# Performance work log

Measured on AMD Instinct MI355X. Metric: run time of the kernel, lower is better.

Reference implementation:

```python
import jax, jax.numpy as jnp
import numpy as np

N_NODES = 10000
EPS = 1e-5


def _layernorm(x, gamma, beta):
    mu = jnp.mean(x, axis=-1, keepdims=True)
    var = jnp.mean(jnp.square(x - mu), axis=-1, keepdims=True)
    return (x - mu) * jax.lax.rsqrt(var + EPS) * gamma + beta


def _sage_pool_layer(h, src, dst, Wp, bp, Ws, Wn, b, gamma, beta):
    # DGL SAGEConv(aggregator='pool'):
    #   m_u = relu(h_u @ Wp^T + bp); h_neigh[v] = max_{u in N(v)} m_u (0 if no neighbors)
    #   rst = h @ Ws^T + h_neigh @ Wn^T + b
    m = jax.nn.relu(h @ Wp.T + bp)              # [N, d]
    msg = m[src]                                 # [E, d] gather
    agg = jax.ops.segment_max(msg, dst, num_segments=N_NODES)
    agg = jnp.where(jnp.isfinite(agg), agg, 0.0)  # isolated nodes -> 0
    rst = h @ Ws.T + agg @ Wn.T + b
    # gsage_layer: LayerNorm, then Encoder applies relu (dropout inactive in eval)
    return jax.nn.relu(_layernorm(rst, gamma, beta))


def setup_inputs() -> dict:
    key = jax.random.key(0)
    ks = jax.random.split(key, 16)
    d = 256
    E = 320000
    s = 1.0 / np.sqrt(d)
    inp = {
        "h": jax.random.normal(ks[0], (N_NODES, d), dtype=jnp.float32),
        "edge_src": jax.random.randint(ks[1], (E,), 0, N_NODES, dtype=jnp.int32),
        "edge_dst": jax.random.randint(ks[2], (E,), 0, N_NODES, dtype=jnp.int32),
    }
    for li in range(2):
        kk = jax.random.split(ks[3 + li], 3)
        inp[f"Wp{li}"] = jax.random.normal(kk[0], (d, d), dtype=jnp.float32) * s
        inp[f"bp{li}"] = jnp.zeros((d,), jnp.float32)
        inp[f"Ws{li}"] = jax.random.normal(kk[1], (d, d), dtype=jnp.float32) * s
        inp[f"Wn{li}"] = jax.random.normal(kk[2], (d, d), dtype=jnp.float32) * s
        inp[f"b{li}"] = jnp.zeros((d,), jnp.float32)
        inp[f"g{li}"] = jnp.ones((d,), jnp.float32)
        inp[f"be{li}"] = jnp.zeros((d,), jnp.float32)
    return inp


def reference(h, edge_src, edge_dst,
              Wp0, bp0, Ws0, Wn0, b0, g0, be0,
              Wp1, bp1, Ws1, Wn1, b1, g1, be1):
    h = _sage_pool_layer(h, edge_src, edge_dst, Wp0, bp0, Ws0, Wn0, b0, g0, be0)
    h = _sage_pool_layer(h, edge_src, edge_dst, Wp1, bp1, Ws1, Wn1, b1, g1, be1)
    return h
```

## Files before the change

kernel.cpp:

```cpp
#include <hip/hip_runtime.h>

#define D 256
#define CAP 128
#define ASTRIDE 280
#define LN_EPS 1e-5f

typedef short short8 __attribute__((ext_vector_type(8)));
typedef float floatx4 __attribute__((ext_vector_type(4)));

__device__ __forceinline__ unsigned short f2b(float f) {
    union { float f; unsigned int u; } x; x.f = f;
    unsigned int u = x.u + 0x7FFFu + ((x.u >> 16) & 1u);
    return (unsigned short)(u >> 16);
}

__global__ __launch_bounds__(256) void prep_kernel(
    const float* __restrict__ w0, const float* __restrict__ w1,
    const float* __restrict__ w2, const float* __restrict__ w3,
    const float* __restrict__ w4, const float* __restrict__ w5,
    unsigned short* __restrict__ wb,
    const float* __restrict__ h, unsigned short* __restrict__ hb, int nh4,
    int* __restrict__ cnt, unsigned short* __restrict__ mb, int N)
{
    const int blk = blockIdx.x;
    const int tid = threadIdx.x;
    if (blk < 384) {
        const int wsel = blk >> 6;
        const float* src;
        switch (wsel) {
            case 0: src = w0; break; case 1: src = w1; break;
            case 2: src = w2; break; case 3: src = w3; break;
            case 4: src = w4; break; default: src = w5; break;
        }
        const int idx = (blk & 63) * 1024 + tid * 4;
        const float4 v = *(const float4*)(src + idx);
        ushort4 o;
        o.x = f2b(v.x); o.y = f2b(v.y); o.z = f2b(v.z); o.w = f2b(v.w);
        *(ushort4*)(wb + (size_t)wsel * 65536 + idx) = o;
    } else if (blk < 1024) {
        int i = (blk - 384) * 256 + tid;
        const int stride = 640 * 256;
        for (; i < nh4; i += stride) {
            const float4 v = *(const float4*)(h + (size_t)i * 4);
            ushort4 o;
            o.x = f2b(v.x); o.y = f2b(v.y); o.z = f2b(v.z); o.w = f2b(v.w);
            *(ushort4*)(hb + (size_t)i * 4) = o;
        }
    } else if (blk < 1064) {
        const int i = (blk - 1024) * 256 + tid;
        if (i < N) cnt[i] = 0;
    } else {
        mb[(size_t)N * D + tid] = 0;
    }
}

__global__ __launch_bounds__(256) void gemm_relu(
    const unsigned short* __restrict__ A, const unsigned short* __restrict__ W,
    const float* __restrict__ bias, unsigned short* __restrict__ out_b, int N,
    const int* __restrict__ esrc, const int* __restrict__ edst,
    int* __restrict__ cnt, int* __restrict__ csr, int E, int ngemm)
{
    if ((int)blockIdx.x >= ngemm) {
        const int nsb = gridDim.x - ngemm;
        int i = ((int)blockIdx.x - ngemm) * 256 + threadIdx.x;
        const int stride = nsb * 256;
        for (; i < E; i += stride) {
            const int d = edst[i];
            const int pos = atomicAdd(&cnt[d], 1);
            if (pos < CAP) csr[(size_t)d * CAP + pos] = esrc[i];
        }
        return;
    }

    const int tid = threadIdx.x;
    const int wave = tid >> 6;
    const int lane = tid & 63;
    const int quad = lane >> 4;
    const int l16 = lane & 15;
    const int row0 = blockIdx.x * 16;
    const int koff = quad * 8;

    floatx4 acc[4];
#pragma unroll
    for (int t = 0; t < 4; t++) acc[t] = (floatx4)(0.f);

    const unsigned short* aptr = A + (size_t)(row0 + l16) * D + koff;
    const unsigned short* wptr = W + (size_t)(wave * 64 + l16) * D + koff;
#pragma unroll
    for (int k0 = 0; k0 < D; k0 += 32) {
        const short8 av = *(const short8*)(aptr + k0);
        const short8 b0 = *(const short8*)(wptr + k0);
        const short8 b1 = *(const short8*)(wptr + 16 * D + k0);
        const short8 b2 = *(const short8*)(wptr + 32 * D + k0);
        const short8 b3 = *(const short8*)(wptr + 48 * D + k0);
        acc[0] = __builtin_amdgcn_mfma_f32_16x16x32_bf16(av, b0, acc[0], 0, 0, 0);
        acc[1] = __builtin_amdgcn_mfma_f32_16x16x32_bf16(av, b1, acc[1], 0, 0, 0);
        acc[2] = __builtin_amdgcn_mfma_f32_16x16x32_bf16(av, b2, acc[2], 0, 0, 0);
        acc[3] = __builtin_amdgcn_mfma_f32_16x16x32_bf16(av, b3, acc[3], 0, 0, 0);
    }

#pragma unroll
    for (int t = 0; t < 4; t++) {
        const float bcol = bias[wave * 64 + t * 16 + l16];
#pragma unroll
        for (int r = 0; r < 4; r++) {
            const int rg = row0 + quad * 4 + r;
            const int col = wave * 64 + t * 16 + l16;
            out_b[(size_t)rg * D + col] = f2b(fmaxf(acc[t][r] + bcol, 0.f));
        }
    }
}

__global__ __launch_bounds__(256, 3) void gemm_ln_pool(
    const unsigned short* __restrict__ A, const unsigned short* __restrict__ Wself,
    const unsigned short* __restrict__ Wneigh,
    const unsigned short* __restrict__ mpool,
    const int* __restrict__ cnt, const int* __restrict__ csr,
    const float* __restrict__ bias,
    const float* __restrict__ gamma, const float* __restrict__ beta,
    unsigned short* __restrict__ out_b, float* __restrict__ out_f, int N)
{
    __shared__ int idxS[16][CAP];
    __shared__ unsigned short aggS[16 * ASTRIDE];
    __shared__ float redS[4][16], redS2[4][16], muA[16], rsA[16];

    const int tid = threadIdx.x;
    const int wave = tid >> 6;
    const int lane = tid & 63;
    const int quad = lane >> 4;
    const int l16 = lane & 15;
    const int row0 = blockIdx.x * 16;
    const int koff = quad * 8;
    const int rbase = wave * 4;

    int degs[4];
#pragma unroll
    for (int rr = 0; rr < 4; rr++) degs[rr] = min(cnt[row0 + rbase + rr], CAP);
    int P = max(max(degs[0], degs[1]), max(degs[2], degs[3]));
    P = (P + 3) & ~3;
#pragma unroll
    for (int rr = 0; rr < 4; rr++) {
        const int rg = row0 + rbase + rr;
        for (int i = lane; i < P; i += 64)
            idxS[rbase + rr][i] = (i < degs[rr]) ? csr[(size_t)rg * CAP + i] : N;
    }

    floatx4 acc[4];
#pragma unroll
    for (int t = 0; t < 4; t++) acc[t] = (floatx4)(0.f);

    {
        const unsigned short* aptr = A + (size_t)(row0 + l16) * D + koff;
        const unsigned short* wptr = Wself + (size_t)(wave * 64 + l16) * D + koff;
#pragma unroll
        for (int k0 = 0; k0 < D; k0 += 32) {
            const short8 av = *(const short8*)(aptr + k0);
            const short8 b0 = *(const short8*)(wptr + k0);
            const short8 b1 = *(const short8*)(wptr + 16 * D + k0);
            const short8 b2 = *(const short8*)(wptr + 32 * D + k0);
            const short8 b3 = *(const short8*)(wptr + 48 * D + k0);
            acc[0] = __builtin_amdgcn_mfma_f32_16x16x32_bf16(av, b0, acc[0], 0, 0, 0);
            acc[1] = __builtin_amdgcn_mfma_f32_16x16x32_bf16(av, b1, acc[1], 0, 0, 0);
            acc[2] = __builtin_amdgcn_mfma_f32_16x16x32_bf16(av, b2, acc[2], 0, 0, 0);
            acc[3] = __builtin_amdgcn_mfma_f32_16x16x32_bf16(av, b3, acc[3], 0, 0, 0);
        }
    }

    {
        ushort4 mx[4];
#pragma unroll
        for (int rr = 0; rr < 4; rr++) { mx[rr].x = 0; mx[rr].y = 0; mx[rr].z = 0; mx[rr].w = 0; }
        for (int i = 0; i < P; i += 4) {
            ushort4 av[4][4];
#pragma unroll
            for (int rr = 0; rr < 4; rr++) {
#pragma unroll
                for (int u = 0; u < 4; u++) {
                    const int j = idxS[rbase + rr][i + u];
                    av[rr][u] = *(const ushort4*)(mpool + (size_t)j * D + lane * 4);
                }
            }
#pragma unroll
            for (int rr = 0; rr < 4; rr++) {
#pragma unroll
                for (int u = 0; u < 4; u++) {
                    mx[rr].x = (unsigned short)max((int)mx[rr].x, (int)av[rr][u].x);
                    mx[rr].y = (unsigned short)max((int)mx[rr].y, (int)av[rr][u].y);
                    mx[rr].z = (unsigned short)max((int)mx[rr].z, (int)av[rr][u].z);
                    mx[rr].w = (unsigned short)max((int)mx[rr].w, (int)av[rr][u].w);
                }
            }
        }
#pragma unroll
        for (int rr = 0; rr < 4; rr++)
            *(ushort4*)&aggS[(rbase + rr) * ASTRIDE + lane * 4] = mx[rr];
    }
    __syncthreads();

    {
        const unsigned short* wptr = Wneigh + (size_t)(wave * 64 + l16) * D + koff;
#pragma unroll
        for (int k0 = 0; k0 < D; k0 += 32) {
            const short8 av = *(const short8*)&aggS[l16 * ASTRIDE + koff + k0];
            const short8 b0 = *(const short8*)(wptr + k0);
            const short8 b1 = *(const short8*)(wptr + 16 * D + k0);
            const short8 b2 = *(const short8*)(wptr + 32 * D + k0);
            const short8 b3 = *(const short8*)(wptr + 48 * D + k0);
            acc[0] = __builtin_amdgcn_mfma_f32_16x16x32_bf16(av, b0, acc[0], 0, 0, 0);
            acc[1] = __builtin_amdgcn_mfma_f32_16x16x32_bf16(av, b1, acc[1], 0, 0, 0);
            acc[2] = __builtin_amdgcn_mfma_f32_16x16x32_bf16(av, b2, acc[2], 0, 0, 0);
            acc[3] = __builtin_amdgcn_mfma_f32_16x16x32_bf16(av, b3, acc[3], 0, 0, 0);
        }
    }

    float bcol[4];
#pragma unroll
    for (int t = 0; t < 4; t++) bcol[t] = bias[wave * 64 + t * 16 + l16];
#pragma unroll
    for (int t = 0; t < 4; t++)
#pragma unroll
        for (int r = 0; r < 4; r++) acc[t][r] += bcol[t];

#pragma unroll
    for (int r = 0; r < 4; r++) {
        float s = 0.f, s2 = 0.f;
#pragma unroll
        for (int t = 0; t < 4; t++) {
            const float v = acc[t][r];
            s += v; s2 += v * v;
        }
        s += __shfl_xor(s, 1);  s2 += __shfl_xor(s2, 1);
        s += __shfl_xor(s, 2);  s2 += __shfl_xor(s2, 2);
        s += __shfl_xor(s, 4);  s2 += __shfl_xor(s2, 4);
        s += __shfl_xor(s, 8);  s2 += __shfl_xor(s2, 8);
        if (l16 == 0) {
            redS[wave][quad * 4 + r] = s;
            redS2[wave][quad * 4 + r] = s2;
        }
    }
    __syncthreads();
    if (tid < 16) {
        const float S  = redS[0][tid] + redS[1][tid] + redS[2][tid] + redS[3][tid];
        const float S2 = redS2[0][tid] + redS2[1][tid] + redS2[2][tid] + redS2[3][tid];
        const float mu = S * (1.f / D);
        float var = S2 * (1.f / D) - mu * mu;
        var = fmaxf(var, 0.f);
        muA[tid] = mu;
        rsA[tid] = rsqrtf(var + LN_EPS);
    }
    __syncthreads();

    float gcol[4], becol[4];
#pragma unroll
    for (int t = 0; t < 4; t++) {
        gcol[t] = gamma[wave * 64 + t * 16 + l16];
        becol[t] = beta[wave * 64 + t * 16 + l16];
    }
#pragma unroll
    for (int r = 0; r < 4; r++) {
        const int rl = quad * 4 + r;
        const int rg = row0 + rl;
        const float mu = muA[rl];
        const float rs = rsA[rl];
#pragma unroll
        for (int t = 0; t < 4; t++) {
            const int col = wave * 64 + t * 16 + l16;
            float o = (acc[t][r] - mu) * rs * gcol[t] + becol[t];
            o = fmaxf(o, 0.f);
            if (out_f) out_f[(size_t)rg * D + col] = o;
            else       out_b[(size_t)rg * D + col] = f2b(o);
        }
    }
}

extern "C" void kernel_launch(void* const* d_in, const int* in_sizes, int n_in,
                              void* d_out, int out_size, void* d_ws, size_t ws_size,
                              hipStream_t stream) {
    const float* h    = (const float*)d_in[0];
    const int*   esrc = (const int*)d_in[1];
    const int*   edst = (const int*)d_in[2];
    const float* Wp0  = (const float*)d_in[3];
    const float* bp0  = (const float*)d_in[4];
    const float* Ws0  = (const float*)d_in[5];
    const float* Wn0  = (const float*)d_in[6];
    const float* b0   = (const float*)d_in[7];
    const float* g0   = (const float*)d_in[8];
    const float* be0  = (const float*)d_in[9];
    const float* Wp1  = (const float*)d_in[10];
    const float* bp1  = (const float*)d_in[11];
    const float* Ws1  = (const float*)d_in[12];
    const float* Wn1  = (const float*)d_in[13];
    const float* b1   = (const float*)d_in[14];
    const float* g1   = (const float*)d_in[15];
    const float* be1  = (const float*)d_in[16];

    const int N = in_sizes[0] / D;
    const int E = in_sizes[1];
    const size_t ND = (size_t)N * D;

    unsigned short* hb  = (unsigned short*)d_ws;
    unsigned short* mb  = hb + ND;
    unsigned short* h1b = mb + ND + D;
    unsigned short* wb  = h1b + ND;
    int* cnt = (int*)(wb + 6 * 65536);
    int* csr = cnt + N;

    unsigned short* wpb0 = wb + 0 * 65536;
    unsigned short* wsb0 = wb + 1 * 65536;
    unsigned short* wnb0 = wb + 2 * 65536;
    unsigned short* wpb1 = wb + 3 * 65536;
    unsigned short* wsb1 = wb + 4 * 65536;
    unsigned short* wnb1 = wb + 5 * 65536;

    const int gblocks = N / 16;
    const int sblocks = 128;

    prep_kernel<<<1065, 256, 0, stream>>>(Wp0, Ws0, Wn0, Wp1, Ws1, Wn1, wb,
                                          h, hb, (int)(ND / 4), cnt, mb, N);

    gemm_relu<<<gblocks + sblocks, 256, 0, stream>>>(hb, wpb0, bp0, mb, N,
                                                     esrc, edst, cnt, csr, E, gblocks);
    gemm_ln_pool<<<gblocks, 256, 0, stream>>>(hb, wsb0, wnb0, mb, cnt, csr,
                                              b0, g0, be0, h1b, nullptr, N);

    gemm_relu<<<gblocks, 256, 0, stream>>>(h1b, wpb1, bp1, mb, N,
                                           esrc, edst, cnt, csr, 0, gblocks);
    gemm_ln_pool<<<gblocks, 256, 0, stream>>>(h1b, wsb1, wnb1, mb, cnt, csr,
                                              b1, g1, be1, nullptr, (float*)d_out, N);
}
```

Before: 234.9 us.

## Compact CSR to u16, double-buffer neighbor max-pool loads and prefetch GEMM operands

Stores CSR neighbor indices as 16-bit values, which halves CSR write/read traffic and the shared index buffer. The max-pool gather is restructured into two ping-pong register bursts of 4x4 loads, with the first burst issued before the self GEMM so its latency overlaps MFMA work. The GEMM loops get explicit one-step register prefetch of the next operands, and the pooling max uses vector u16 max. It relies on node IDs fitting in 16 bits (N=10000) and raises register pressure, which may reduce occupancy.

```diff
diff --git a/kernel.cpp b/kernel.cpp
--- a/kernel.cpp
+++ b/kernel.cpp
@@ -7,6 +7,18 @@
 
 typedef short short8 __attribute__((ext_vector_type(8)));
 typedef float floatx4 __attribute__((ext_vector_type(4)));
+typedef unsigned short u16x4 __attribute__((ext_vector_type(4)));
+
+__device__ __forceinline__ u16x4 umax4(u16x4 a, u16x4 b) {
+#if __has_builtin(__builtin_elementwise_max)
+    return __builtin_elementwise_max(a, b);
+#else
+    u16x4 r;
+    r.x = a.x > b.x ? a.x : b.x; r.y = a.y > b.y ? a.y : b.y;
+    r.z = a.z > b.z ? a.z : b.z; r.w = a.w > b.w ? a.w : b.w;
+    return r;
+#endif
+}
 
 __device__ __forceinline__ unsigned short f2b(float f) {
     union { float f; unsigned int u; } x; x.f = f;
@@ -58,7 +70,7 @@
     const unsigned short* __restrict__ A, const unsigned short* __restrict__ W,
     const float* __restrict__ bias, unsigned short* __restrict__ out_b, int N,
     const int* __restrict__ esrc, const int* __restrict__ edst,
-    int* __restrict__ cnt, int* __restrict__ csr, int E, int ngemm)
+    int* __restrict__ cnt, unsigned short* __restrict__ csr, int E, int ngemm)
 {
     if ((int)blockIdx.x >= ngemm) {
         const int nsb = gridDim.x - ngemm;
@@ -67,7 +79,7 @@
         for (; i < E; i += stride) {
             const int d = edst[i];
             const int pos = atomicAdd(&cnt[d], 1);
-            if (pos < CAP) csr[(size_t)d * CAP + pos] = esrc[i];
+            if (pos < CAP) csr[(size_t)d * CAP + pos] = (unsigned short)esrc[i];
         }
         return;
     }
@@ -86,17 +98,29 @@
 
     const unsigned short* aptr = A + (size_t)(row0 + l16) * D + koff;
     const unsigned short* wptr = W + (size_t)(wave * 64 + l16) * D + koff;
+
+    short8 a_c  = *(const short8*)(aptr);
+    short8 b_c0 = *(const short8*)(wptr);
+    short8 b_c1 = *(const short8*)(wptr + 16 * D);
+    short8 b_c2 = *(const short8*)(wptr + 32 * D);
+    short8 b_c3 = *(const short8*)(wptr + 48 * D);
 #pragma unroll
     for (int k0 = 0; k0 < D; k0 += 32) {
-        const short8 av = *(const short8*)(aptr + k0);
-        const short8 b0 = *(const short8*)(wptr + k0);
-        const short8 b1 = *(const short8*)(wptr + 16 * D + k0);
-        const short8 b2 = *(const short8*)(wptr + 32 * D + k0);
-        const short8 b3 = *(const short8*)(wptr + 48 * D + k0);
-        acc[0] = __builtin_amdgcn_mfma_f32_16x16x32_bf16(av, b0, acc[0], 0, 0, 0);
-        acc[1] = __builtin_amdgcn_mfma_f32_16x16x32_bf16(av, b1, acc[1], 0, 0, 0);
-        acc[2] = __builtin_amdgcn_mfma_f32_16x16x32_bf16(av, b2, acc[2], 0, 0, 0);
-        acc[3] = __builtin_amdgcn_mfma_f32_16x16x32_bf16(av, b3, acc[3], 0, 0, 0);
+        short8 a_n, b_n0, b_n1, b_n2, b_n3;
+        if (k0 + 32 < D) {
+            a_n  = *(const short8*)(aptr + k0 + 32);
+            b_n0 = *(const short8*)(wptr + k0 + 32);
+            b_n1 = *(const short8*)(wptr + 16 * D + k0 + 32);
+            b_n2 = *(const short8*)(wptr + 32 * D + k0 + 32);
+            b_n3 = *(const short8*)(wptr + 48 * D + k0 + 32);
+        }
+        acc[0] = __builtin_amdgcn_mfma_f32_16x16x32_bf16(a_c, b_c0, acc[0], 0, 0, 0);
+        acc[1] = __builtin_amdgcn_mfma_f32_16x16x32_bf16(a_c, b_c1, acc[1], 0, 0, 0);
+        acc[2] = __builtin_amdgcn_mfma_f32_16x16x32_bf16(a_c, b_c2, acc[2], 0, 0, 0);
+        acc[3] = __builtin_amdgcn_mfma_f32_16x16x32_bf16(a_c, b_c3, acc[3], 0, 0, 0);
+        if (k0 + 32 < D) {
+            a_c = a_n; b_c0 = b_n0; b_c1 = b_n1; b_c2 = b_n2; b_c3 = b_n3;
+        }
     }
 
 #pragma unroll
@@ -115,12 +139,12 @@
     const unsigned short* __restrict__ A, const unsigned short* __restrict__ Wself,
     const unsigned short* __restrict__ Wneigh,
     const unsigned short* __restrict__ mpool,
-    const int* __restrict__ cnt, const int* __restrict__ csr,
+    const int* __restrict__ cnt, const unsigned short* __restrict__ csr,
     const float* __restrict__ bias,
     const float* __restrict__ gamma, const float* __restrict__ beta,
     unsigned short* __restrict__ out_b, float* __restrict__ out_f, int N)
 {
-    __shared__ int idxS[16][CAP];
+    __shared__ unsigned short idxS[16][CAP];
     __shared__ unsigned short aggS[16 * ASTRIDE];
     __shared__ float redS[4][16], redS2[4][16], muA[16], rsA[16];
 
@@ -137,13 +161,37 @@
 #pragma unroll
     for (int rr = 0; rr < 4; rr++) degs[rr] = min(cnt[row0 + rbase + rr], CAP);
     int P = max(max(degs[0], degs[1]), max(degs[2], degs[3]));
-    P = (P + 3) & ~3;
+    const int P8 = (P + 7) & ~7;
 #pragma unroll
     for (int rr = 0; rr < 4; rr++) {
         const int rg = row0 + rbase + rr;
-        for (int i = lane; i < P; i += 64)
-            idxS[rbase + rr][i] = (i < degs[rr]) ? csr[(size_t)rg * CAP + i] : N;
-    }
+        for (int i = lane; i < P8; i += 64)
+            idxS[rbase + rr][i] = (i < degs[rr]) ? csr[(size_t)rg * CAP + i]
+                                                 : (unsigned short)N;
+    }
+
+    const unsigned short* mrow = mpool + lane * 4;
+    u16x4 bufA[4][4], bufB[4][4];
+    u16x4 mx[4];
+#pragma unroll
+    for (int rr = 0; rr < 4; rr++) mx[rr] = (u16x4)(0);
+
+#define LOAD_BURST(buf, i0)                                                     \
+    {                                                                           \
+        _Pragma("unroll") for (int rr = 0; rr < 4; rr++)                        \
+        _Pragma("unroll") for (int u = 0; u < 4; u++)                           \
+            buf[rr][u] = *(const u16x4*)(mrow +                                 \
+                (size_t)idxS[rbase + rr][(i0) + u] * D);                        \
+    }
+#define CONS_BURST(buf)                                                         \
+    {                                                                           \
+        _Pragma("unroll") for (int rr = 0; rr < 4; rr++)                        \
+            mx[rr] = umax4(mx[rr],                                              \
+                umax4(umax4(buf[rr][0], buf[rr][1]),                            \
+                      umax4(buf[rr][2], buf[rr][3])));                          \
+    }
+
+    if (P8 > 0) LOAD_BURST(bufA, 0);
 
     floatx4 acc[4];
 #pragma unroll
@@ -152,64 +200,71 @@
     {
         const unsigned short* aptr = A + (size_t)(row0 + l16) * D + koff;
         const unsigned short* wptr = Wself + (size_t)(wave * 64 + l16) * D + koff;
+        short8 a_c  = *(const short8*)(aptr);
+        short8 b_c0 = *(const short8*)(wptr);
+        short8 b_c1 = *(const short8*)(wptr + 16 * D);
+        short8 b_c2 = *(const short8*)(wptr + 32 * D);
+        short8 b_c3 = *(const short8*)(wptr + 48 * D);
 #pragma unroll
         for (int k0 = 0; k0 < D; k0 += 32) {
-            const short8 av = *(const short8*)(aptr + k0);
-            const short8 b0 = *(const short8*)(wptr + k0);
-            const short8 b1 = *(const short8*)(wptr + 16 * D + k0);
-            const short8 b2 = *(const short8*)(wptr + 32 * D + k0);
-            const short8 b3 = *(const short8*)(wptr + 48 * D + k0);
-            acc[0] = __builtin_amdgcn_mfma_f32_16x16x32_bf16(av, b0, acc[0], 0, 0, 0);
-            acc[1] = __builtin_amdgcn_mfma_f32_16x16x32_bf16(av, b1, acc[1], 0, 0, 0);
-            acc[2] = __builtin_amdgcn_mfma_f32_16x16x32_bf16(av, b2, acc[2], 0, 0, 0);
-            acc[3] = __builtin_amdgcn_mfma_f32_16x16x32_bf16(av, b3, acc[3], 0, 0, 0);
-        }
-    }
-
-    {
-        ushort4 mx[4];
-#pragma unroll
-        for (int rr = 0; rr < 4; rr++) { mx[rr].x = 0; mx[rr].y = 0; mx[rr].z = 0; mx[rr].w = 0; }
-        for (int i = 0; i < P; i += 4) {
-            ushort4 av[4][4];
-#pragma unroll
-            for (int rr = 0; rr < 4; rr++) {
-#pragma unroll
-                for (int u = 0; u < 4; u++) {
-                    const int j = idxS[rbase + rr][i + u];
-                    av[rr][u] = *(const ushort4*)(mpool + (size_t)j * D + lane * 4);
-                }
+            short8 a_n, b_n0, b_n1, b_n2, b_n3;
+            if (k0 + 32 < D) {
+                a_n  = *(const short8*)(aptr + k0 + 32);
+                b_n0 = *(const short8*)(wptr + k0 + 32);
+                b_n1 = *(const short8*)(wptr + 16 * D + k0 + 32);
+                b_n2 = *(const short8*)(wptr + 32 * D + k0 + 32);
+                b_n3 = *(const short8*)(wptr + 48 * D + k0 + 32);
             }
-#pragma unroll
-            for (int rr = 0; rr < 4; rr++) {
-#pragma unroll
-                for (int u = 0; u < 4; u++) {
-                    mx[rr].x = (unsigned short)max((int)mx[rr].x, (int)av[rr][u].x);
-                    mx[rr].y = (unsigned short)max((int)mx[rr].y, (int)av[rr][u].y);
-                    mx[rr].z = (unsigned short)max((int)mx[rr].z, (int)av[rr][u].z);
-                    mx[rr].w = (unsigned short)max((int)mx[rr].w, (int)av[rr][u].w);
-                }
+            acc[0] = __builtin_amdgcn_mfma_f32_16x16x32_bf16(a_c, b_c0, acc[0], 0, 0, 0);
+            acc[1] = __builtin_amdgcn_mfma_f32_16x16x32_bf16(a_c, b_c1, acc[1], 0, 0, 0);
+            acc[2] = __builtin_amdgcn_mfma_f32_16x16x32_bf16(a_c, b_c2, acc[2], 0, 0, 0);
+            acc[3] = __builtin_amdgcn_mfma_f32_16x16x32_bf16(a_c, b_c3, acc[3], 0, 0, 0);
+            if (k0 + 32 < D) {
+                a_c = a_n; b_c0 = b_n0; b_c1 = b_n1; b_c2 = b_n2; b_c3 = b_n3;
             }
         }
-#pragma unroll
-        for (int rr = 0; rr < 4; rr++)
-            *(ushort4*)&aggS[(rbase + rr) * ASTRIDE + lane * 4] = mx[rr];
-    }
+    }
+
+    if (P8 > 0) {
+        LOAD_BURST(bufB, 4);
+        for (int i = 8; i < P8; i += 8) {
+            CONS_BURST(bufA);
+            LOAD_BURST(bufA, i);
+            CONS_BURST(bufB);
+            LOAD_BURST(bufB, i + 4);
+        }
+        CONS_BURST(bufA);
+        CONS_BURST(bufB);
+    }
+#pragma unroll
+    for (int rr = 0; rr < 4; rr++)
+        *(u16x4*)&aggS[(rbase + rr) * ASTRIDE + lane * 4] = mx[rr];
     __syncthreads();
 
     {
         const unsigned short* wptr = Wneigh + (size_t)(wave * 64 + l16) * D + koff;
+        short8 a_c  = *(const short8*)&aggS[l16 * ASTRIDE + koff];
+        short8 b_c0 = *(const short8*)(wptr);
+        short8 b_c1 = *(const short8*)(wptr + 16 * D);
+        short8 b_c2 = *(const short8*)(wptr + 32 * D);
+        short8 b_c3 = *(const short8*)(wptr + 48 * D);
 #pragma unroll
         for (int k0 = 0; k0 < D; k0 += 32) {
-            const short8 av = *(const short8*)&aggS[l16 * ASTRIDE + koff + k0];
-            const short8 b0 = *(const short8*)(wptr + k0);
-            const short8 b1 = *(const short8*)(wptr + 16 * D + k0);
-            const short8 b2 = *(const short8*)(wptr + 32 * D + k0);
-            const short8 b3 = *(const short8*)(wptr + 48 * D + k0);
-            acc[0] = __builtin_amdgcn_mfma_f32_16x16x32_bf16(av, b0, acc[0], 0, 0, 0);
-            acc[1] = __builtin_amdgcn_mfma_f32_16x16x32_bf16(av, b1, acc[1], 0, 0, 0);
-            acc[2] = __builtin_amdgcn_mfma_f32_16x16x32_bf16(av, b2, acc[2], 0, 0, 0);
-            acc[3] = __builtin_amdgcn_mfma_f32_16x16x32_bf16(av, b3, acc[3], 0, 0, 0);
+            short8 a_n, b_n0, b_n1, b_n2, b_n3;
+            if (k0 + 32 < D) {
+                a_n  = *(const short8*)&aggS[l16 * ASTRIDE + koff + k0 + 32];
+                b_n0 = *(const short8*)(wptr + k0 + 32);
+                b_n1 = *(const short8*)(wptr + 16 * D + k0 + 32);
+                b_n2 = *(const short8*)(wptr + 32 * D + k0 + 32);
+                b_n3 = *(const short8*)(wptr + 48 * D + k0 + 32);
+            }
+            acc[0] = __builtin_amdgcn_mfma_f32_16x16x32_bf16(a_c, b_c0, acc[0], 0, 0, 0);
+            acc[1] = __builtin_amdgcn_mfma_f32_16x16x32_bf16(a_c, b_c1, acc[1], 0, 0, 0);
+            acc[2] = __builtin_amdgcn_mfma_f32_16x16x32_bf16(a_c, b_c2, acc[2], 0, 0, 0);
+            acc[3] = __builtin_amdgcn_mfma_f32_16x16x32_bf16(a_c, b_c3, acc[3], 0, 0, 0);
+            if (k0 + 32 < D) {
+                a_c = a_n; b_c0 = b_n0; b_c1 = b_n1; b_c2 = b_n2; b_c3 = b_n3;
+            }
         }
     }
 
@@ -303,7 +358,7 @@
     unsigned short* h1b = mb + ND + D;
     unsigned short* wb  = h1b + ND;
     int* cnt = (int*)(wb + 6 * 65536);
-    int* csr = cnt + N;
+    unsigned short* csr = (unsigned short*)(cnt + N);
 
     unsigned short* wpb0 = wb + 0 * 65536;
     unsigned short* wsb0 = wb + 1 * 65536;
```

After: 237.4 us. About the same (+1.1%).

## Bucket neighbor lists by source chunk with 16-bit indices for pooled gather

Applied to the files above, without the earlier changes.

The per-destination neighbor list is split into four buckets keyed by which 2560-row chunk the source node falls in. Each bucket holds 16-bit source indices instead of 32-bit, and the max-pooling gather walks the buckets in order. This aims to improve cache locality of the gathered message rows and to halve the index storage and traffic. The max reduction is also rewritten with vector elementwise max. In exchange, each bucket is padded separately, which adds extra padded gathers per row group. The scheme also depends on N fitting in 16 bits and on a hardcoded block bound in the prep kernel.

```diff
diff --git a/kernel.cpp b/kernel.cpp
--- a/kernel.cpp
+++ b/kernel.cpp
@@ -1,12 +1,26 @@
 #include <hip/hip_runtime.h>
 
 #define D 256
-#define CAP 128
+#define NCHUNK 4
+#define CHUNK_ROWS 2560
+#define CAP4 64
 #define ASTRIDE 280
 #define LN_EPS 1e-5f
 
 typedef short short8 __attribute__((ext_vector_type(8)));
 typedef float floatx4 __attribute__((ext_vector_type(4)));
+typedef unsigned short u16x4 __attribute__((ext_vector_type(4)));
+
+__device__ __forceinline__ u16x4 umax4(u16x4 a, u16x4 b) {
+#if __has_builtin(__builtin_elementwise_max)
+    return __builtin_elementwise_max(a, b);
+#else
+    u16x4 r;
+    r.x = a.x > b.x ? a.x : b.x; r.y = a.y > b.y ? a.y : b.y;
+    r.z = a.z > b.z ? a.z : b.z; r.w = a.w > b.w ? a.w : b.w;
+    return r;
+#endif
+}
 
 __device__ __forceinline__ unsigned short f2b(float f) {
     union { float f; unsigned int u; } x; x.f = f;
@@ -46,9 +60,9 @@
             o.x = f2b(v.x); o.y = f2b(v.y); o.z = f2b(v.z); o.w = f2b(v.w);
             *(ushort4*)(hb + (size_t)i * 4) = o;
         }
-    } else if (blk < 1064) {
+    } else if (blk < 1181) {
         const int i = (blk - 1024) * 256 + tid;
-        if (i < N) cnt[i] = 0;
+        if (i < N * NCHUNK) cnt[i] = 0;
     } else {
         mb[(size_t)N * D + tid] = 0;
     }
@@ -58,7 +72,7 @@
     const unsigned short* __restrict__ A, const unsigned short* __restrict__ W,
     const float* __restrict__ bias, unsigned short* __restrict__ out_b, int N,
     const int* __restrict__ esrc, const int* __restrict__ edst,
-    int* __restrict__ cnt, int* __restrict__ csr, int E, int ngemm)
+    int* __restrict__ cnt, unsigned short* __restrict__ csr, int E, int ngemm)
 {
     if ((int)blockIdx.x >= ngemm) {
         const int nsb = gridDim.x - ngemm;
@@ -66,8 +80,11 @@
         const int stride = nsb * 256;
         for (; i < E; i += stride) {
             const int d = edst[i];
-            const int pos = atomicAdd(&cnt[d], 1);
-            if (pos < CAP) csr[(size_t)d * CAP + pos] = esrc[i];
+            const int s = esrc[i];
+            const int ch = s / CHUNK_ROWS;
+            const int pos = atomicAdd(&cnt[d * NCHUNK + ch], 1);
+            if (pos < CAP4)
+                csr[((size_t)d * NCHUNK + ch) * CAP4 + pos] = (unsigned short)s;
         }
         return;
     }
@@ -115,12 +132,12 @@
     const unsigned short* __restrict__ A, const unsigned short* __restrict__ Wself,
     const unsigned short* __restrict__ Wneigh,
     const unsigned short* __restrict__ mpool,
-    const int* __restrict__ cnt, const int* __restrict__ csr,
+    const int* __restrict__ cnt, const unsigned short* __restrict__ csr,
     const float* __restrict__ bias,
     const float* __restrict__ gamma, const float* __restrict__ beta,
     unsigned short* __restrict__ out_b, float* __restrict__ out_f, int N)
 {
-    __shared__ int idxS[16][CAP];
+    __shared__ unsigned short idxS[16][NCHUNK][CAP4];
     __shared__ unsigned short aggS[16 * ASTRIDE];
     __shared__ float redS[4][16], redS2[4][16], muA[16], rsA[16];
 
@@ -133,16 +150,22 @@
     const int koff = quad * 8;
     const int rbase = wave * 4;
 
-    int degs[4];
-#pragma unroll
-    for (int rr = 0; rr < 4; rr++) degs[rr] = min(cnt[row0 + rbase + rr], CAP);
-    int P = max(max(degs[0], degs[1]), max(degs[2], degs[3]));
-    P = (P + 3) & ~3;
-#pragma unroll
-    for (int rr = 0; rr < 4; rr++) {
-        const int rg = row0 + rbase + rr;
-        for (int i = lane; i < P; i += 64)
-            idxS[rbase + rr][i] = (i < degs[rr]) ? csr[(size_t)rg * CAP + i] : N;
+    int P4[NCHUNK];
+#pragma unroll
+    for (int ch = 0; ch < NCHUNK; ch++) {
+        int degs[4];
+#pragma unroll
+        for (int rr = 0; rr < 4; rr++)
+            degs[rr] = min(cnt[(row0 + rbase + rr) * NCHUNK + ch], CAP4);
+        int P = max(max(degs[0], degs[1]), max(degs[2], degs[3]));
+        P4[ch] = (P + 3) & ~3;
+#pragma unroll
+        for (int rr = 0; rr < 4; rr++) {
+            const size_t base = ((size_t)(row0 + rbase + rr) * NCHUNK + ch) * CAP4;
+            for (int i = lane; i < P4[ch]; i += 64)
+                idxS[rbase + rr][ch][i] = (i < degs[rr]) ? csr[base + i]
+                                                         : (unsigned short)N;
+        }
     }
 
     floatx4 acc[4];
@@ -167,33 +190,33 @@
     }
 
     {
-        ushort4 mx[4];
-#pragma unroll
-        for (int rr = 0; rr < 4; rr++) { mx[rr].x = 0; mx[rr].y = 0; mx[rr].z = 0; mx[rr].w = 0; }
-        for (int i = 0; i < P; i += 4) {
-            ushort4 av[4][4];
-#pragma unroll
-            for (int rr = 0; rr < 4; rr++) {
-#pragma unroll
-                for (int u = 0; u < 4; u++) {
-                    const int j = idxS[rbase + rr][i + u];
-                    av[rr][u] = *(const ushort4*)(mpool + (size_t)j * D + lane * 4);
+        const unsigned short* mrow = mpool + lane * 4;
+        u16x4 mx[4];
+#pragma unroll
+        for (int rr = 0; rr < 4; rr++) mx[rr] = (u16x4)(0);
+#pragma unroll
+        for (int ch = 0; ch < NCHUNK; ch++) {
+            const int P = P4[ch];
+            for (int i = 0; i < P; i += 4) {
+                u16x4 av[4][4];
+#pragma unroll
+                for (int rr = 0; rr < 4; rr++) {
+#pragma unroll
+                    for (int u = 0; u < 4; u++) {
+                        const int j = idxS[rbase + rr][ch][i + u];
+                        av[rr][u] = *(const u16x4*)(mrow + (size_t)j * D);
+                    }
                 }
+#pragma unroll
+                for (int rr = 0; rr < 4; rr++)
+                    mx[rr] = umax4(mx[rr],
+                             umax4(umax4(av[rr][0], av[rr][1]),
+                                   umax4(av[rr][2], av[rr][3])));
             }
-#pragma unroll
-            for (int rr = 0; rr < 4; rr++) {
-#pragma unroll
-                for (int u = 0; u < 4; u++) {
-                    mx[rr].x = (unsigned short)max((int)mx[rr].x, (int)av[rr][u].x);
-                    mx[rr].y = (unsigned short)max((int)mx[rr].y, (int)av[rr][u].y);
-                    mx[rr].z = (unsigned short)max((int)mx[rr].z, (int)av[rr][u].z);
-                    mx[rr].w = (unsigned short)max((int)mx[rr].w, (int)av[rr][u].w);
-                }
-            }
         }
 #pragma unroll
         for (int rr = 0; rr < 4; rr++)
-            *(ushort4*)&aggS[(rbase + rr) * ASTRIDE + lane * 4] = mx[rr];
+            *(u16x4*)&aggS[(rbase + rr) * ASTRIDE + lane * 4] = mx[rr];
     }
     __syncthreads();
 
@@ -303,7 +326,7 @@
     unsigned short* h1b = mb + ND + D;
     unsigned short* wb  = h1b + ND;
     int* cnt = (int*)(wb + 6 * 65536);
-    int* csr = cnt + N;
+    unsigned short* csr = (unsigned short*)(cnt + (size_t)N * NCHUNK);
 
     unsigned short* wpb0 = wb + 0 * 65536;
     unsigned short* wsb0 = wb + 1 * 65536;
@@ -314,9 +337,11 @@
 
     const int gblocks = N / 16;
     const int sblocks = 128;
-
-    prep_kernel<<<1065, 256, 0, stream>>>(Wp0, Ws0, Wn0, Wp1, Ws1, Wn1, wb,
-                                          h, hb, (int)(ND / 4), cnt, mb, N);
+    const int zblocks = (N * NCHUNK + 255) / 256;
+    const int pgrid = 1024 + zblocks + 1;
+
+    prep_kernel<<<pgrid, 256, 0, stream>>>(Wp0, Ws0, Wn0, Wp1, Ws1, Wn1, wb,
+                                           h, hb, (int)(ND / 4), cnt, mb, N);
 
     gemm_relu<<<gblocks + sblocks, 256, 0, stream>>>(hb, wpb0, bp0, mb, N,
                                                      esrc, edst, cnt, csr, E, gblocks);
```

After: 244.8 us. +4.2%, slower.

## Gather pool messages via async global_load_lds double buffering with 16-bit CSR indices

Applied to the files above, without the earlier changes.

Replaces the register-based neighbor gather in the pooling max with asynchronous global-to-LDS loads into a per-wave double buffer, so the next burst of neighbor rows is fetched while the current one is being reduced. Neighbor indices are stored as 16-bit values in the CSR and in shared memory, which halves the index traffic. The LDS footprint grows with the gather buffers, which may lower occupancy. The 16-bit indices only hold while N stays at or below 65535.

```diff
diff --git a/kernel.cpp b/kernel.cpp
--- a/kernel.cpp
+++ b/kernel.cpp
@@ -7,6 +7,23 @@
 
 typedef short short8 __attribute__((ext_vector_type(8)));
 typedef float floatx4 __attribute__((ext_vector_type(4)));
+typedef unsigned short u16x4 __attribute__((ext_vector_type(4)));
+
+typedef const __attribute__((address_space(1))) void* gas_t;
+typedef __attribute__((address_space(3))) void* las_t;
+
+#define WAIT_VM(n) __builtin_amdgcn_s_waitcnt(((n) & 0xF) | (((n) >> 4) << 14) | (7 << 4) | (0xF << 8))
+
+__device__ __forceinline__ u16x4 umax4(u16x4 a, u16x4 b) {
+#if __has_builtin(__builtin_elementwise_max)
+    return __builtin_elementwise_max(a, b);
+#else
+    u16x4 r;
+    r.x = a.x > b.x ? a.x : b.x; r.y = a.y > b.y ? a.y : b.y;
+    r.z = a.z > b.z ? a.z : b.z; r.w = a.w > b.w ? a.w : b.w;
+    return r;
+#endif
+}
 
 __device__ __forceinline__ unsigned short f2b(float f) {
     union { float f; unsigned int u; } x; x.f = f;
@@ -58,7 +75,7 @@
     const unsigned short* __restrict__ A, const unsigned short* __restrict__ W,
     const float* __restrict__ bias, unsigned short* __restrict__ out_b, int N,
     const int* __restrict__ esrc, const int* __restrict__ edst,
-    int* __restrict__ cnt, int* __restrict__ csr, int E, int ngemm)
+    int* __restrict__ cnt, unsigned short* __restrict__ csr, int E, int ngemm)
 {
     if ((int)blockIdx.x >= ngemm) {
         const int nsb = gridDim.x - ngemm;
@@ -67,7 +84,7 @@
         for (; i < E; i += stride) {
             const int d = edst[i];
             const int pos = atomicAdd(&cnt[d], 1);
-            if (pos < CAP) csr[(size_t)d * CAP + pos] = esrc[i];
+            if (pos < CAP) csr[(size_t)d * CAP + pos] = (unsigned short)esrc[i];
         }
         return;
     }
@@ -115,12 +132,13 @@
     const unsigned short* __restrict__ A, const unsigned short* __restrict__ Wself,
     const unsigned short* __restrict__ Wneigh,
     const unsigned short* __restrict__ mpool,
-    const int* __restrict__ cnt, const int* __restrict__ csr,
+    const int* __restrict__ cnt, const unsigned short* __restrict__ csr,
     const float* __restrict__ bias,
     const float* __restrict__ gamma, const float* __restrict__ beta,
     unsigned short* __restrict__ out_b, float* __restrict__ out_f, int N)
 {
-    __shared__ int idxS[16][CAP];
+    __shared__ unsigned short idxS[16][CAP];
+    __shared__ unsigned short gbuf[4][2][8][D];
     __shared__ unsigned short aggS[16 * ASTRIDE];
     __shared__ float redS[4][16], redS2[4][16], muA[16], rsA[16];
 
@@ -132,17 +150,20 @@
     const int row0 = blockIdx.x * 16;
     const int koff = quad * 8;
     const int rbase = wave * 4;
+    const int half = lane >> 5;
+    const int l32 = lane & 31;
 
     int degs[4];
 #pragma unroll
     for (int rr = 0; rr < 4; rr++) degs[rr] = min(cnt[row0 + rbase + rr], CAP);
     int P = max(max(degs[0], degs[1]), max(degs[2], degs[3]));
-    P = (P + 3) & ~3;
+    const int P2 = (P + 1) & ~1;
 #pragma unroll
     for (int rr = 0; rr < 4; rr++) {
         const int rg = row0 + rbase + rr;
-        for (int i = lane; i < P; i += 64)
-            idxS[rbase + rr][i] = (i < degs[rr]) ? csr[(size_t)rg * CAP + i] : N;
+        for (int i = lane; i < P2; i += 64)
+            idxS[rbase + rr][i] = (i < degs[rr]) ? csr[(size_t)rg * CAP + i]
+                                                 : (unsigned short)N;
     }
 
     floatx4 acc[4];
@@ -167,33 +188,38 @@
     }
 
     {
-        ushort4 mx[4];
-#pragma unroll
-        for (int rr = 0; rr < 4; rr++) { mx[rr].x = 0; mx[rr].y = 0; mx[rr].z = 0; mx[rr].w = 0; }
-        for (int i = 0; i < P; i += 4) {
-            ushort4 av[4][4];
+        const int nb = P2 >> 1;
+        u16x4 mx[4];
+#pragma unroll
+        for (int rr = 0; rr < 4; rr++) mx[rr] = (u16x4)(0);
+
+#define ISSUE_BURST(bi, buf)                                                    \
+        {                                                                       \
+            _Pragma("unroll") for (int rr = 0; rr < 4; rr++) {                  \
+                const int jj = idxS[rbase + rr][2 * (bi) + half];               \
+                const unsigned short* g = mpool + (size_t)jj * D + l32 * 8;     \
+                __builtin_amdgcn_global_load_lds(                               \
+                    (gas_t)g, (las_t)&gbuf[wave][buf][rr * 2][0], 16, 0, 0);    \
+            }                                                                   \
+        }
+
+        if (nb > 0) ISSUE_BURST(0, 0);
+        if (nb > 1) ISSUE_BURST(1, 1);
+        for (int b = 0; b < nb; b++) {
+            if (b + 1 < nb) WAIT_VM(4); else WAIT_VM(0);
+            const int buf = b & 1;
 #pragma unroll
             for (int rr = 0; rr < 4; rr++) {
-#pragma unroll
-                for (int u = 0; u < 4; u++) {
-                    const int j = idxS[rbase + rr][i + u];
-                    av[rr][u] = *(const ushort4*)(mpool + (size_t)j * D + lane * 4);
-                }
+                const u16x4 a0 = *(const u16x4*)&gbuf[wave][buf][rr * 2 + 0][lane * 4];
+                const u16x4 a1 = *(const u16x4*)&gbuf[wave][buf][rr * 2 + 1][lane * 4];
+                mx[rr] = umax4(mx[rr], umax4(a0, a1));
             }
-#pragma unroll
-            for (int rr = 0; rr < 4; rr++) {
-#pragma unroll
-                for (int u = 0; u < 4; u++) {
-                    mx[rr].x = (unsigned short)max((int)mx[rr].x, (int)av[rr][u].x);
-                    mx[rr].y = (unsigned short)max((int)mx[rr].y, (int)av[rr][u].y);
-                    mx[rr].z = (unsigned short)max((int)mx[rr].z, (int)av[rr][u].z);
-                    mx[rr].w = (unsigned short)max((int)mx[rr].w, (int)av[rr][u].w);
-                }
-            }
-        }
+            if (b + 2 < nb) ISSUE_BURST(b + 2, buf);
+        }
+#undef ISSUE_BURST
 #pragma unroll
         for (int rr = 0; rr < 4; rr++)
-            *(ushort4*)&aggS[(rbase + rr) * ASTRIDE + lane * 4] = mx[rr];
+            *(u16x4*)&aggS[(rbase + rr) * ASTRIDE + lane * 4] = mx[rr];
     }
     __syncthreads();
 
@@ -303,7 +329,7 @@
     unsigned short* h1b = mb + ND + D;
     unsigned short* wb  = h1b + ND;
     int* cnt = (int*)(wb + 6 * 65536);
-    int* csr = cnt + N;
+    unsigned short* csr = (unsigned short*)(cnt + N);
 
     unsigned short* wpb0 = wb + 0 * 65536;
     unsigned short* wsb0 = wb + 1 * 65536;
```

Result: faster. 222.2 us (-5.4%).
